# Optimization experiments

Measured on AMD Instinct MI355X. Metric: run time of the kernel, lower is better.

## Reference

```python
import jax, jax.numpy as jnp
import numpy as np

N_NODES = 20000
N_EDGES = 160000
D = 1000          # out_channels of GatedGraphConv / Linear in-dim
NUM_LAYERS = 3


def setup_inputs() -> dict:
    key = jax.random.key(0)
    ks = jax.random.split(key, 10)
    x = jax.random.normal(ks[0], (N_NODES, D), dtype=jnp.float32)
    edge_index = jax.random.randint(ks[1], (2, N_EDGES), 0, N_NODES, dtype=jnp.int32)
    edge_weight = jax.random.uniform(ks[2], (N_EDGES,), dtype=jnp.float32)
    s = 1.0 / np.sqrt(D)
    weight = jax.random.uniform(ks[3], (NUM_LAYERS, D, D), minval=-s, maxval=s, dtype=jnp.float32)
    w_ih = jax.random.uniform(ks[4], (3 * D, D), minval=-s, maxval=s, dtype=jnp.float32)
    w_hh = jax.random.uniform(ks[5], (3 * D, D), minval=-s, maxval=s, dtype=jnp.float32)
    b_ih = jax.random.uniform(ks[6], (3 * D,), minval=-s, maxval=s, dtype=jnp.float32)
    b_hh = jax.random.uniform(ks[7], (3 * D,), minval=-s, maxval=s, dtype=jnp.float32)
    fc_w = jax.random.uniform(ks[8], (1, D), minval=-s, maxval=s, dtype=jnp.float32)
    fc_b = jax.random.uniform(ks[9], (1,), minval=-s, maxval=s, dtype=jnp.float32)
    return {
        "x": x, "edge_index": edge_index, "edge_weight": edge_weight,
        "weight": weight, "w_ih": w_ih, "w_hh": w_hh, "b_ih": b_ih, "b_hh": b_hh,
        "fc_w": fc_w, "fc_b": fc_b, "prob": 0,
    }


def _gru_cell(m, h, w_ih, w_hh, b_ih, b_hh):
    # torch.nn.GRUCell: gate order r, z, n
    gi = m @ w_ih.T + b_ih   # [N, 3D]
    gh = h @ w_hh.T + b_hh   # [N, 3D]
    i_r, i_z, i_n = jnp.split(gi, 3, axis=-1)
    h_r, h_z, h_n = jnp.split(gh, 3, axis=-1)
    r = jax.nn.sigmoid(i_r + h_r)
    z = jax.nn.sigmoid(i_z + h_z)
    n = jnp.tanh(i_n + r * h_n)
    return (1.0 - z) * n + z * h


def reference(x, edge_index, edge_weight, weight, w_ih, w_hh, b_ih, b_hh, fc_w, fc_b, prob):
    src = edge_index[0]
    dst = edge_index[1]
    h = x
    for layer in range(NUM_LAYERS):
        m = h @ weight[layer]                                  # [N, D]
        msg = m[src] * edge_weight[:, None]                    # [E, D]
        agg = jax.ops.segment_sum(msg, dst, num_segments=N_NODES)  # scatter-add
        h = _gru_cell(agg, h, w_ih, w_hh, b_ih, b_hh)
    h = jax.nn.relu(h)
    # F.dropout with p=prob=0 is identity (scale 1/(1-0)=1)
    return h @ fc_w.T + fc_b                                   # [N, 1]
```

## Files before the change

kernel.cpp:

```cpp
#include <hip/hip_runtime.h>

typedef unsigned short u16;
typedef unsigned int u32;
typedef __attribute__((ext_vector_type(8))) short bf16x8;
typedef __attribute__((ext_vector_type(4))) float f32x4;

#define N_NODES 20000
#define N_EDGES 160000
#define DDIM    1000
#define KP      1024
#define SP      41200000
#define WCAT_L  6291456

__device__ __forceinline__ float b2f(u16 u) {
    union { u32 i; float f; } v; v.i = ((u32)u) << 16; return v.f;
}
__device__ __forceinline__ u16 f2b(float f) {
    union { float f; u32 i; } v; v.f = f;
    u32 r = v.i + 0x7FFFu + ((v.i >> 16) & 1u);
    return (u16)(r >> 16);
}
__device__ __forceinline__ u32 pack2(float a, float b) {
    return (u32)f2b(a) | ((u32)f2b(b) << 16);
}
__device__ __forceinline__ f32x4 mfma16(bf16x8 a, bf16x8 b, f32x4 c) {
    return __builtin_amdgcn_mfma_f32_16x16x32_bf16(a, b, c, 0, 0, 0);
}
__device__ __forceinline__ float fexp_(float x) {
    return __builtin_amdgcn_exp2f(x * 1.4426950408889634f);
}
__device__ __forceinline__ float fsigmoid_(float x) {
    return __builtin_amdgcn_rcpf(1.0f + fexp_(-x));
}
__device__ __forceinline__ float ftanh_(float x) {
    float ax = fabsf(x);
    float e = fexp_(-2.0f * ax);
    float t = (1.0f - e) * __builtin_amdgcn_rcpf(1.0f + e);
    return x >= 0.0f ? t : -t;
}

__device__ __forceinline__ void gl2lds16(const u16* g, u16* l) {
    __builtin_amdgcn_global_load_lds(
        (const __attribute__((address_space(1))) u32*)g,
        (__attribute__((address_space(3))) u32*)l, 16, 0, 0);
}

__global__ __launch_bounds__(256) void cvt_rows(const float* __restrict__ in,
                                                u16* __restrict__ out) {
    int r = blockIdx.x, c = threadIdx.x * 4;
    u32 o[2] = {0, 0};
    if (c < DDIM) {
        float4 v = *(const float4*)(in + (size_t)r * DDIM + c);
        o[0] = pack2(v.x, v.y); o[1] = pack2(v.z, v.w);
    }
    *(uint2*)(out + (size_t)r * KP + c) = *(const uint2*)o;
}

__global__ __launch_bounds__(256) void cvt_wb3(const float* __restrict__ W,
                                               u16* __restrict__ Wb3) {
    int r = blockIdx.x, l = blockIdx.y, c = threadIdx.x * 4;
    const float* in = W + (size_t)l * 1000000 + (size_t)r * DDIM;
    u32 o[2] = {0, 0};
    if (c < DDIM) {
        float4 v = *(const float4*)(in + c);
        o[0] = pack2(v.x, v.y); o[1] = pack2(v.z, v.w);
    }
    *(uint2*)(Wb3 + (size_t)l * 1048576 + (size_t)r * KP + c) = *(const uint2*)o;
}

__global__ __launch_bounds__(256) void cvt_whh3(const float* __restrict__ whh,
                                                u16* __restrict__ wcat) {
    int r = blockIdx.x, l = blockIdx.y, c = threadIdx.x * 4;
    int g = r / 1000, n = r - g * 1000;
    u32 o[2] = {0, 0};
    if (c < DDIM) {
        float4 v = *(const float4*)(whh + (size_t)r * DDIM + c);
        o[0] = pack2(v.x, v.y); o[1] = pack2(v.z, v.w);
    }
    u16* dst = wcat + (size_t)l * WCAT_L + ((size_t)g * 1024 + n) * 2048 + 1024;
    *(uint2*)(dst + c) = *(const uint2*)o;
}

__global__ __launch_bounds__(256) void count_edges(const int* __restrict__ ei,
                                                   int* __restrict__ cnt) {
    int e = blockIdx.x * 256 + threadIdx.x;
    if (e < N_EDGES) atomicAdd(&cnt[ei[N_EDGES + e]], 1);
}

__global__ __launch_bounds__(1024) void scan_offsets(const int* __restrict__ cnt,
                                                     int* __restrict__ ofs) {
    __shared__ int s[1024];
    const int CH = 20;
    int t = threadIdx.x;
    int base = t * CH;
    int loc[CH];
    int sum = 0;
    for (int j = 0; j < CH; j++) {
        int i = base + j;
        loc[j] = sum;
        sum += (i < N_NODES) ? cnt[i] : 0;
    }
    s[t] = sum;
    __syncthreads();
    for (int d = 1; d < 1024; d <<= 1) {
        int v = (t >= d) ? s[t - d] : 0;
        __syncthreads();
        s[t] += v;
        __syncthreads();
    }
    int excl = s[t] - sum;
    for (int j = 0; j < CH; j++) {
        int i = base + j;
        if (i < N_NODES) ofs[i] = excl + loc[j];
    }
    if (t == 0) ofs[N_NODES] = N_EDGES;
}

__global__ __launch_bounds__(256) void fill_buckets(const int* __restrict__ ei,
                                                    const int* __restrict__ ofs,
                                                    int* __restrict__ cur,
                                                    int* __restrict__ bkt) {
    int e = blockIdx.x * 256 + threadIdx.x;
    if (e >= N_EDGES) return;
    int d = ei[N_EDGES + e];
    int pos = atomicAdd(&cur[d], 1);
    bkt[ofs[d] + pos] = e;
}

__global__ __launch_bounds__(256) void node_agg(const int* __restrict__ ei,
                                                const float* __restrict__ ew,
                                                const int* __restrict__ ofs,
                                                const int* __restrict__ bkt,
                                                const u16* __restrict__ hsrc,
                                                u16* __restrict__ agg) {
    __shared__ int   s_src[64];
    __shared__ float s_w[64];
    int node = blockIdx.x;
    int t = threadIdx.x;
    int beg = ofs[node], end = ofs[node + 1];
    float4 acc = {0.f, 0.f, 0.f, 0.f};
    for (int cb = beg; cb < end; cb += 64) {
        int n = min(64, end - cb);
        if (t < n) {
            int e = bkt[cb + t];
            s_src[t] = ei[e];
            s_w[t]   = ew[e];
        }
        __syncthreads();
        if (t < 250) {
            for (int j = 0; j < n; j++) {
                int src = s_src[j];
                float w = s_w[j];
                uint2 v = *(const uint2*)(hsrc + (size_t)src * KP + t * 4);
                const u16* p = (const u16*)&v;
                acc.x += b2f(p[0]) * w;
                acc.y += b2f(p[1]) * w;
                acc.z += b2f(p[2]) * w;
                acc.w += b2f(p[3]) * w;
            }
        }
        __syncthreads();
    }
    if (t < 250) {
        u32 o[2] = {pack2(acc.x, acc.y), pack2(acc.z, acc.w)};
        *(uint2*)(agg + (size_t)node * KP + t * 4) = *(const uint2*)o;
    } else {
        uint2 z = {0, 0};
        *(uint2*)(agg + (size_t)node * KP + 1000 + (t - 250) * 4) = z;
    }
}

__global__ __launch_bounds__(256) void gemm_wc(const u16* __restrict__ A,
                                               const u16* __restrict__ Bt3,
                                               u16* __restrict__ wcat) {
    __shared__ u16 S[16384];
    int tid = threadIdx.x;
    int lane = tid & 63, wave = tid >> 6;
    int wr = wave >> 1, wc = wave & 1;
    int bid = blockIdx.x;
    int l = blockIdx.y;
    int m0 = (bid >> 3) * 128, n0 = (bid & 7) * 128;
    const u16* Bt = Bt3 + (size_t)l * 1048576;

    int aoff[4], boff[4];
#pragma unroll
    for (int i = 0; i < 4; i++) {
        int c = tid + 256 * i;
        int row = c >> 3, sl = c & 7;
        int kc = sl ^ (row & 7);
        aoff[i] = (m0 + row) * KP + kc * 8;
        boff[i] = (n0 + row) * KP + kc * 8;
    }
    f32x4 acc[4][4] = {};
    int fr = lane & 15, q = lane >> 4, sw = fr & 7;

    for (int k0 = 0; k0 < KP; k0 += 64) {
#pragma unroll
        for (int i = 0; i < 4; i++) {
            gl2lds16(A + aoff[i] + k0, &S[tid * 8 + 2048 * i]);
            gl2lds16(Bt + boff[i] + k0, &S[8192 + tid * 8 + 2048 * i]);
        }
        __syncthreads();
#pragma unroll
        for (int ks = 0; ks < 2; ks++) {
            int kx = ((ks * 4 + q) ^ sw) * 8;
            bf16x8 af[4], bf[4];
#pragma unroll
            for (int i = 0; i < 4; i++)
                af[i] = *(const bf16x8*)&S[(wr * 64 + i * 16 + fr) * 64 + kx];
#pragma unroll
            for (int j = 0; j < 4; j++)
                bf[j] = *(const bf16x8*)&S[8192 + (wc * 64 + j * 16 + fr) * 64 + kx];
#pragma unroll
            for (int i = 0; i < 4; i++)
#pragma unroll
                for (int j = 0; j < 4; j++)
                    acc[i][j] = mfma16(af[i], bf[j], acc[i][j]);
        }
        __syncthreads();
    }

    u16* wl = wcat + (size_t)l * WCAT_L;
    int cc = lane & 15, r4 = q * 4;
#pragma unroll
    for (int i = 0; i < 4; i++)
#pragma unroll
        for (int j = 0; j < 4; j++) {
            int gn = n0 + wc * 64 + j * 16 + cc;
            if (gn >= DDIM) continue;
#pragma unroll
            for (int r = 0; r < 4; r++) {
                int gm = m0 + wr * 64 + i * 16 + r4 + r;
                if (gm >= 3000) continue;
                int slab = (gm >= 2000) ? 2 : (gm >= 1000 ? 1 : 0);
                int row = gm - slab * 1000;
                wl[(size_t)slab * 2097152 + (size_t)row * 2048 + gn] =
                    f2b(acc[i][j][r]);
            }
        }
}

__global__ __launch_bounds__(256) void gru_fused(const u16* __restrict__ agg,
                                                 const u16* __restrict__ h,
                                                 const u16* __restrict__ wcat,
                                                 const float* __restrict__ bih,
                                                 const float* __restrict__ bhh,
                                                 u16* __restrict__ hout) {
    __shared__ u16 S[20480];
    int tid = threadIdx.x;
    int lane = tid & 63, wave = tid >> 6;
    int wr = wave >> 1, wc = wave & 1;

    int bid = blockIdx.x;
    int xcd = bid & 7;
    int s = bid >> 3;
    int hi = (s >= 157) ? 1 : 0;
    int m0 = (s - hi * 157) * 128;
    int n0 = (xcd * 2 + hi) * 64;

    int aoff[4], woff[2];
#pragma unroll
    for (int i = 0; i < 4; i++) {
        int c = tid + 256 * i;
        int row = c >> 3, sl = c & 7;
        int kc = sl ^ (row & 7);
        aoff[i] = (m0 + row) * KP + kc * 8;
    }
#pragma unroll
    for (int i = 0; i < 2; i++) {
        int c = tid + 256 * i;
        int row = (c >> 3) & 63, sl = c & 7;
        int kc = sl ^ (row & 7);
        woff[i] = (n0 + row) * 2048 + kc * 8;
    }
    f32x4 aR[4][2] = {}, aZ[4][2] = {}, aN[4][2] = {}, aH[4][2] = {};
    int fr = lane & 15, q = lane >> 4, sw = fr & 7;

#define GRU_PHASE(APTR, K0W, AN)                                              \
    for (int kk = 0; kk < 16; kk++) {                                         \
        int ka = kk * 64, kw = K0W + kk * 64;                                 \
        _Pragma("unroll")                                                     \
        for (int i = 0; i < 4; i++)                                           \
            gl2lds16(APTR + aoff[i] + ka, &S[tid * 8 + 2048 * i]);            \
        _Pragma("unroll")                                                     \
        for (int i = 0; i < 2; i++) {                                         \
            gl2lds16(wcat + woff[i] + kw, &S[8192 + tid * 8 + 2048 * i]);     \
            gl2lds16(wcat + 2097152 + woff[i] + kw,                           \
                     &S[12288 + tid * 8 + 2048 * i]);                         \
            gl2lds16(wcat + 4194304 + woff[i] + kw,                           \
                     &S[16384 + tid * 8 + 2048 * i]);                         \
        }                                                                     \
        __syncthreads();                                                      \
        _Pragma("unroll")                                                     \
        for (int ks = 0; ks < 2; ks++) {                                      \
            int kx = ((ks * 4 + q) ^ sw) * 8;                                 \
            bf16x8 aa[4], w0[2], w1[2], w2[2];                                \
            _Pragma("unroll")                                                 \
            for (int i = 0; i < 4; i++)                                       \
                aa[i] = *(const bf16x8*)&S[(wr * 64 + i * 16 + fr) * 64 + kx];\
            _Pragma("unroll")                                                 \
            for (int j = 0; j < 2; j++) {                                     \
                int rb = (wc * 32 + j * 16 + fr) * 64 + kx;                   \
                w0[j] = *(const bf16x8*)&S[8192 + rb];                        \
                w1[j] = *(const bf16x8*)&S[12288 + rb];                       \
                w2[j] = *(const bf16x8*)&S[16384 + rb];                       \
            }                                                                 \
            _Pragma("unroll")                                                 \
            for (int i = 0; i < 4; i++)                                       \
                _Pragma("unroll")                                             \
                for (int j = 0; j < 2; j++) {                                 \
                    aR[i][j] = mfma16(aa[i], w0[j], aR[i][j]);                \
                    aZ[i][j] = mfma16(aa[i], w1[j], aZ[i][j]);                \
                    AN[i][j] = mfma16(aa[i], w2[j], AN[i][j]);                \
                }                                                             \
        }                                                                     \
        __syncthreads();                                                      \
    }

    GRU_PHASE(agg, 0, aN)
    GRU_PHASE(h, 1024, aH)
#undef GRU_PHASE

    int cc = lane & 15, r4 = q * 4;
#pragma unroll
    for (int j = 0; j < 2; j++) {
        int gn = n0 + wc * 32 + j * 16 + cc;
        if (gn >= DDIM) continue;
        float br  = bih[gn] + bhh[gn];
        float bz  = bih[1000 + gn] + bhh[1000 + gn];
        float bni = bih[2000 + gn];
        float bnh = bhh[2000 + gn];
#pragma unroll
        for (int i = 0; i < 4; i++)
#pragma unroll
            for (int r = 0; r < 4; r++) {
                int gm = m0 + wr * 64 + i * 16 + r4 + r;
                if (gm >= N_NODES) continue;
                float rg = fsigmoid_(aR[i][j][r] + br);
                float zg = fsigmoid_(aZ[i][j][r] + bz);
                float ng = ftanh_(aN[i][j][r] + bni + rg * (aH[i][j][r] + bnh));
                size_t idx = (size_t)gm * KP + gn;
                float hp = b2f(h[idx]);
                hout[idx] = f2b((1.0f - zg) * ng + zg * hp);
            }
    }
}

__global__ __launch_bounds__(256) void fc_out(const u16* __restrict__ h,
                                              const float* __restrict__ fw,
                                              const float* __restrict__ fb,
                                              float* __restrict__ out) {
    int row = blockIdx.x * 4 + (threadIdx.x >> 6);
    int lane = threadIdx.x & 63;
    if (row >= N_NODES) return;
    float s = 0.0f;
    for (int i = 0; i < 4; i++) {
        int c = lane + 64 * i;
        if (c < 250) {
            uint2 v = *(const uint2*)(h + (size_t)row * KP + c * 4);
            float4 w = *(const float4*)(fw + c * 4);
            const u16* pv = (const u16*)&v;
            float h0 = b2f(pv[0]), h1 = b2f(pv[1]), h2 = b2f(pv[2]), h3 = b2f(pv[3]);
            s += (h0 > 0.0f ? h0 : 0.0f) * w.x;
            s += (h1 > 0.0f ? h1 : 0.0f) * w.y;
            s += (h2 > 0.0f ? h2 : 0.0f) * w.z;
            s += (h3 > 0.0f ? h3 : 0.0f) * w.w;
        }
    }
    for (int off = 32; off > 0; off >>= 1) s += __shfl_down(s, off, 64);
    if (lane == 0) out[row] = s + fb[0];
}

extern "C" void kernel_launch(void* const* d_in, const int* in_sizes, int n_in,
                              void* d_out, int out_size, void* d_ws, size_t ws_size,
                              hipStream_t stream) {
    const float* x   = (const float*)d_in[0];
    const int*   ei  = (const int*)d_in[1];
    const float* ew  = (const float*)d_in[2];
    const float* W   = (const float*)d_in[3];
    const float* wih = (const float*)d_in[4];
    const float* whh = (const float*)d_in[5];
    const float* bih = (const float*)d_in[6];
    const float* bhh = (const float*)d_in[7];
    const float* fw  = (const float*)d_in[8];
    const float* fb  = (const float*)d_in[9];
    float* out = (float*)d_out;

    char* ws = (char*)d_ws;
    u16* xb   = (u16*)(ws);
    u16* bufA = (u16*)(ws + (size_t)SP);
    u16* bufB = (u16*)(ws + (size_t)2 * SP);
    u16* wcat = (u16*)(ws + 123600000);
    int* cnt  = (int*)(ws + 161400000);
    int* cur  = (int*)(ws + 161500000);
    int* ofs  = (int*)(ws + 161600000);
    int* bkt  = (int*)(ws + 161700096);

    u16* wihb = bufA;
    u16* Wb3  = bufA + 3145728;

    cvt_rows<<<N_NODES, 256, 0, stream>>>(x, xb);
    cvt_rows<<<3000, 256, 0, stream>>>(wih, wihb);
    cvt_wb3<<<dim3(1000, 3), 256, 0, stream>>>(W, Wb3);
    gemm_wc<<<dim3(192, 3), 256, 0, stream>>>(wihb, Wb3, wcat);
    cvt_whh3<<<dim3(3000, 3), 256, 0, stream>>>(whh, wcat);
    hipMemsetAsync(cnt, 0, 80000, stream);
    hipMemsetAsync(cur, 0, 80000, stream);
    count_edges<<<625, 256, 0, stream>>>(ei, cnt);
    scan_offsets<<<1, 1024, 0, stream>>>(cnt, ofs);
    fill_buckets<<<625, 256, 0, stream>>>(ei, ofs, cur, bkt);

    node_agg<<<N_NODES, 256, 0, stream>>>(ei, ew, ofs, bkt, xb, bufB);
    gru_fused<<<2512, 256, 0, stream>>>(bufB, xb, wcat, bih, bhh, bufA);

    node_agg<<<N_NODES, 256, 0, stream>>>(ei, ew, ofs, bkt, bufA, bufB);
    gru_fused<<<2512, 256, 0, stream>>>(bufB, bufA, wcat + WCAT_L, bih, bhh, xb);

    node_agg<<<N_NODES, 256, 0, stream>>>(ei, ew, ofs, bkt, xb, bufB);
    gru_fused<<<2512, 256, 0, stream>>>(bufB, xb, wcat + 2 * WCAT_L, bih, bhh, bufA);

    fc_out<<<5000, 256, 0, stream>>>(bufA, fw, fb, out);
}
```

Measured before the change: 1.273 ms.

## Widen node aggregation loads, process two nodes per block, merge weight conversions

node_agg now handles two destination nodes per 256-thread block, with 128 threads per node each doing 16-byte loads of eight bf16 values, where before each thread did 8-byte loads. The three weight-conversion kernels are merged into one launch, and the two counter memsets become one by placing cnt and cur next to each other. fc_out also switches to 16-byte loads. The aim is fewer memory instructions and fewer launches, at the cost of idle threads in a block when the two nodes' degrees differ.

```diff
diff --git a/kernel.cpp b/kernel.cpp
--- a/kernel.cpp
+++ b/kernel.cpp
@@ -56,28 +56,35 @@
     *(uint2*)(out + (size_t)r * KP + c) = *(const uint2*)o;
 }
 
-__global__ __launch_bounds__(256) void cvt_wb3(const float* __restrict__ W,
-                                               u16* __restrict__ Wb3) {
-    int r = blockIdx.x, l = blockIdx.y, c = threadIdx.x * 4;
-    const float* in = W + (size_t)l * 1000000 + (size_t)r * DDIM;
+__global__ __launch_bounds__(256) void cvt_weights(const float* __restrict__ wih,
+                                                   const float* __restrict__ W,
+                                                   const float* __restrict__ whh,
+                                                   u16* __restrict__ wihb,
+                                                   u16* __restrict__ Wb3,
+                                                   u16* __restrict__ wcat) {
+    int b = blockIdx.x, c = threadIdx.x * 4;
+    const float* src;
+    u16* dst;
+    if (b < 3000) {
+        src = wih + (size_t)b * DDIM;
+        dst = wihb + (size_t)b * KP;
+    } else if (b < 6000) {
+        int r = b - 3000;
+        int l = r / 1000, row = r - l * 1000;
+        src = W + (size_t)r * DDIM;
+        dst = Wb3 + (size_t)l * 1048576 + (size_t)row * KP;
+    } else {
+        int r = b - 6000;
+        int l = r / 3000, gr = r - l * 3000;
+        int g = gr / 1000, n2 = gr - g * 1000;
+        src = whh + (size_t)gr * DDIM;
+        dst = wcat + (size_t)l * WCAT_L + ((size_t)g * 1024 + n2) * 2048 + 1024;
+    }
     u32 o[2] = {0, 0};
     if (c < DDIM) {
-        float4 v = *(const float4*)(in + c);
+        float4 v = *(const float4*)(src + c);
         o[0] = pack2(v.x, v.y); o[1] = pack2(v.z, v.w);
     }
-    *(uint2*)(Wb3 + (size_t)l * 1048576 + (size_t)r * KP + c) = *(const uint2*)o;
-}
-
-__global__ __launch_bounds__(256) void cvt_whh3(const float* __restrict__ whh,
-                                                u16* __restrict__ wcat) {
-    int r = blockIdx.x, l = blockIdx.y, c = threadIdx.x * 4;
-    int g = r / 1000, n = r - g * 1000;
-    u32 o[2] = {0, 0};
-    if (c < DDIM) {
-        float4 v = *(const float4*)(whh + (size_t)r * DDIM + c);
-        o[0] = pack2(v.x, v.y); o[1] = pack2(v.z, v.w);
-    }
-    u16* dst = wcat + (size_t)l * WCAT_L + ((size_t)g * 1024 + n) * 2048 + 1024;
     *(uint2*)(dst + c) = *(const uint2*)o;
 }
 
@@ -133,40 +140,45 @@
                                                 const int* __restrict__ bkt,
                                                 const u16* __restrict__ hsrc,
                                                 u16* __restrict__ agg) {
-    __shared__ int   s_src[64];
-    __shared__ float s_w[64];
-    int node = blockIdx.x;
-    int t = threadIdx.x;
+    __shared__ int   s_src[2][32];
+    __shared__ float s_w[2][32];
+    __shared__ int   s_it[2];
+    int tid = threadIdx.x;
+    int half = tid >> 7, t = tid & 127;
+    int node = blockIdx.x * 2 + half;
     int beg = ofs[node], end = ofs[node + 1];
-    float4 acc = {0.f, 0.f, 0.f, 0.f};
-    for (int cb = beg; cb < end; cb += 64) {
-        int n = min(64, end - cb);
+    if (t == 0) s_it[half] = (end - beg + 31) >> 5;
+    __syncthreads();
+    int iters = max(s_it[0], s_it[1]);
+    float acc[8] = {};
+    for (int it = 0; it < iters; it++) {
+        int cb = beg + it * 32;
+        int n = min(32, end - cb);
         if (t < n) {
             int e = bkt[cb + t];
-            s_src[t] = ei[e];
-            s_w[t]   = ew[e];
-        }
-        __syncthreads();
-        if (t < 250) {
+            s_src[half][t] = ei[e];
+            s_w[half][t]   = ew[e];
+        }
+        __syncthreads();
+        if (t < 125) {
             for (int j = 0; j < n; j++) {
-                int src = s_src[j];
-                float w = s_w[j];
-                uint2 v = *(const uint2*)(hsrc + (size_t)src * KP + t * 4);
+                int src = s_src[half][j];
+                float w = s_w[half][j];
+                uint4 v = *(const uint4*)(hsrc + (size_t)src * KP + t * 8);
                 const u16* p = (const u16*)&v;
-                acc.x += b2f(p[0]) * w;
-                acc.y += b2f(p[1]) * w;
-                acc.z += b2f(p[2]) * w;
-                acc.w += b2f(p[3]) * w;
+#pragma unroll
+                for (int k = 0; k < 8; k++) acc[k] += b2f(p[k]) * w;
             }
         }
         __syncthreads();
     }
-    if (t < 250) {
-        u32 o[2] = {pack2(acc.x, acc.y), pack2(acc.z, acc.w)};
-        *(uint2*)(agg + (size_t)node * KP + t * 4) = *(const uint2*)o;
-    } else {
-        uint2 z = {0, 0};
-        *(uint2*)(agg + (size_t)node * KP + 1000 + (t - 250) * 4) = z;
+    if (t < 125) {
+        u32 o[4] = {pack2(acc[0], acc[1]), pack2(acc[2], acc[3]),
+                    pack2(acc[4], acc[5]), pack2(acc[6], acc[7])};
+        *(uint4*)(agg + (size_t)node * KP + t * 8) = *(const uint4*)o;
+    } else if (t < 128) {
+        uint4 z = {0, 0, 0, 0};
+        *(uint4*)(agg + (size_t)node * KP + 1000 + (t - 125) * 8) = z;
     }
 }
 
@@ -354,17 +366,27 @@
     int lane = threadIdx.x & 63;
     if (row >= N_NODES) return;
     float s = 0.0f;
-    for (int i = 0; i < 4; i++) {
+#pragma unroll
+    for (int i = 0; i < 2; i++) {
         int c = lane + 64 * i;
-        if (c < 250) {
-            uint2 v = *(const uint2*)(h + (size_t)row * KP + c * 4);
-            float4 w = *(const float4*)(fw + c * 4);
+        if (c < 125) {
+            uint4 v = *(const uint4*)(h + (size_t)row * KP + c * 8);
             const u16* pv = (const u16*)&v;
-            float h0 = b2f(pv[0]), h1 = b2f(pv[1]), h2 = b2f(pv[2]), h3 = b2f(pv[3]);
-            s += (h0 > 0.0f ? h0 : 0.0f) * w.x;
-            s += (h1 > 0.0f ? h1 : 0.0f) * w.y;
-            s += (h2 > 0.0f ? h2 : 0.0f) * w.z;
-            s += (h3 > 0.0f ? h3 : 0.0f) * w.w;
+            float4 w0 = *(const float4*)(fw + c * 8);
+            float4 w1 = *(const float4*)(fw + c * 8 + 4);
+            const float* wp = (const float*)&w0;
+            float hv;
+#pragma unroll
+            for (int k = 0; k < 4; k++) {
+                hv = b2f(pv[k]);
+                s += (hv > 0.0f ? hv : 0.0f) * wp[k];
+            }
+            wp = (const float*)&w1;
+#pragma unroll
+            for (int k = 0; k < 4; k++) {
+                hv = b2f(pv[4 + k]);
+                s += (hv > 0.0f ? hv : 0.0f) * wp[k];
+            }
         }
     }
     for (int off = 32; off > 0; off >>= 1) s += __shfl_down(s, off, 64);
@@ -392,31 +414,28 @@
     u16* bufB = (u16*)(ws + (size_t)2 * SP);
     u16* wcat = (u16*)(ws + 123600000);
     int* cnt  = (int*)(ws + 161400000);
-    int* cur  = (int*)(ws + 161500000);
-    int* ofs  = (int*)(ws + 161600000);
-    int* bkt  = (int*)(ws + 161700096);
+    int* cur  = (int*)(ws + 161480000);
+    int* ofs  = (int*)(ws + 161560000);
+    int* bkt  = (int*)(ws + 161640192);
 
     u16* wihb = bufA;
     u16* Wb3  = bufA + 3145728;
 
     cvt_rows<<<N_NODES, 256, 0, stream>>>(x, xb);
-    cvt_rows<<<3000, 256, 0, stream>>>(wih, wihb);
-    cvt_wb3<<<dim3(1000, 3), 256, 0, stream>>>(W, Wb3);
+    cvt_weights<<<15000, 256, 0, stream>>>(wih, W, whh, wihb, Wb3, wcat);
     gemm_wc<<<dim3(192, 3), 256, 0, stream>>>(wihb, Wb3, wcat);
-    cvt_whh3<<<dim3(3000, 3), 256, 0, stream>>>(whh, wcat);
-    hipMemsetAsync(cnt, 0, 80000, stream);
-    hipMemsetAsync(cur, 0, 80000, stream);
+    hipMemsetAsync(cnt, 0, 160000, stream);
     count_edges<<<625, 256, 0, stream>>>(ei, cnt);
     scan_offsets<<<1, 1024, 0, stream>>>(cnt, ofs);
     fill_buckets<<<625, 256, 0, stream>>>(ei, ofs, cur, bkt);
 
-    node_agg<<<N_NODES, 256, 0, stream>>>(ei, ew, ofs, bkt, xb, bufB);
+    node_agg<<<10000, 256, 0, stream>>>(ei, ew, ofs, bkt, xb, bufB);
     gru_fused<<<2512, 256, 0, stream>>>(bufB, xb, wcat, bih, bhh, bufA);
 
-    node_agg<<<N_NODES, 256, 0, stream>>>(ei, ew, ofs, bkt, bufA, bufB);
+    node_agg<<<10000, 256, 0, stream>>>(ei, ew, ofs, bkt, bufA, bufB);
     gru_fused<<<2512, 256, 0, stream>>>(bufB, bufA, wcat + WCAT_L, bih, bhh, xb);
 
-    node_agg<<<N_NODES, 256, 0, stream>>>(ei, ew, ofs, bkt, xb, bufB);
+    node_agg<<<10000, 256, 0, stream>>>(ei, ew, ofs, bkt, xb, bufB);
     gru_fused<<<2512, 256, 0, stream>>>(bufB, xb, wcat + 2 * WCAT_L, bih, bhh, bufA);
 
     fc_out<<<5000, 256, 0, stream>>>(bufA, fw, fb, out);
```

Result: no change. 1.272 ms (-0.1%).
